# Kernel optimization log

Measured on AMD Instinct MI355X. Metric: run time of the kernel, lower is better.

## Reference

```python
import jax, jax.numpy as jnp
import numpy as np

N, B, M = 262144, 4, 32
C3D, C2D, MID, OUT = 64, 256, 128, 64
H, W = 96, 312
VOXEL_SIZE = jnp.array([0.05, 0.05, 0.1], dtype=jnp.float32)
PC_RANGE = jnp.array([0.0, -40.0, -3.0], dtype=jnp.float32)
CLASS_W3D = jnp.array([0.85, 0.95, 0.6], dtype=jnp.float32)  # Car, Pedestrian, Cyclist
DEFAULT_W3D = 0.8
EPS = 1e-5

def _bn(x, g, b, m, v):
    # eval-mode batchnorm
    return (x - m) * jax.lax.rsqrt(v + EPS) * g + b

def setup_inputs():
    key = jax.random.key(0)
    ks = jax.random.split(key, 16)
    vb = jax.random.randint(ks[0], (N,), 0, B)
    vz = jax.random.randint(ks[1], (N,), 0, 40)
    vy = jax.random.randint(ks[2], (N,), 0, 1600)
    vx = jax.random.randint(ks[3], (N,), 0, 1408)
    voxel_coords = jnp.stack([vb, vz, vy, vx], axis=1).astype(jnp.int32)
    voxel_features = jax.random.normal(ks[4], (N, C3D), dtype=jnp.float32)
    image_features = jax.random.normal(ks[5], (B, C2D, H, W), dtype=jnp.float32)
    cxy = jax.random.uniform(ks[6], (B, M, 2)) * jnp.array([70.4, 80.0]) + jnp.array([0.0, -40.0])
    cz = jax.random.uniform(ks[7], (B, M, 1)) * 4.0 - 3.0
    dims = jax.random.uniform(ks[8], (B, M, 3)) * 3.0 + 1.0
    yaw = jax.random.uniform(ks[9], (B, M, 1)) * 6.28
    gt_boxes = jnp.concatenate([cxy, cz, dims, yaw], axis=-1).astype(jnp.float32)
    gt_classes = jax.random.randint(ks[10], (B, M), 0, 3)
    def lin(k, o, i):
        return (jax.random.normal(k, (o, i), dtype=jnp.float32) / np.float32(np.sqrt(i)))
    return dict(
        voxel_features=voxel_features, voxel_coords=voxel_coords,
        image_features=image_features, gt_boxes=gt_boxes, gt_classes=gt_classes,
        w_vt=lin(ks[11], MID, C3D), b_vt=jnp.zeros(MID),
        g_vt=jnp.ones(MID), be_vt=jnp.zeros(MID), m_vt=jnp.zeros(MID), v_vt=jnp.ones(MID),
        w_it=lin(ks[12], MID, C2D), b_it=jnp.zeros(MID),
        g_it=jnp.ones(MID), be_it=jnp.zeros(MID), m_it=jnp.zeros(MID), v_it=jnp.ones(MID),
        w_f=lin(ks[13], OUT, 2 * MID), b_f=jnp.zeros(OUT),
        g_f=jnp.ones(OUT), be_f=jnp.zeros(OUT), m_f=jnp.zeros(OUT), v_f=jnp.ones(OUT),
    )

def reference(voxel_features, voxel_coords, image_features, gt_boxes, gt_classes,
              w_vt, b_vt, g_vt, be_vt, m_vt, v_vt,
              w_it, b_it, g_it, be_it, m_it, v_it,
              w_f, b_f, g_f, be_f, m_f, v_f):
    b_idx = voxel_coords[:, 0]
    xyz = jnp.stack([voxel_coords[:, 3], voxel_coords[:, 2], voxel_coords[:, 1]], axis=1).astype(jnp.float32)
    centers_raw = xyz * VOXEL_SIZE + PC_RANGE            # class-aware path (no half-voxel offset)
    centers = centers_raw + VOXEL_SIZE * 0.5             # sampling path

    # voxel transform: Linear + BN + ReLU
    vt = jax.nn.relu(_bn(voxel_features @ w_vt.T + b_vt, g_vt, be_vt, m_vt, v_vt))

    # image transform: 1x1 conv + BN + ReLU over all images at once
    it = jnp.einsum('oc,bchw->bohw', w_it, image_features) + b_it[None, :, None, None]
    it = jax.nn.relu(_bn(it, g_it[None, :, None, None], be_it[None, :, None, None],
                         m_it[None, :, None, None], v_it[None, :, None, None]))

    # fallback projection (no calib): xy*10 + [W/2, H/2], normalize to [-1,1], clamp
    px = centers[:, 0] * 10.0 + W / 2.0
    py = centers[:, 1] * 10.0 + H / 2.0
    nx = jnp.clip(px / W * 2.0 - 1.0, -1.0, 1.0)
    ny = jnp.clip(py / H * 2.0 - 1.0, -1.0, 1.0)
    # grid_sample bilinear, align_corners=False, zero padding
    fx = ((nx + 1.0) * W - 1.0) * 0.5
    fy = ((ny + 1.0) * H - 1.0) * 0.5
    x0 = jnp.floor(fx); y0 = jnp.floor(fy)

    def gather(xi, yi):
        valid = (xi >= 0) & (xi < W) & (yi >= 0) & (yi < H)
        xc = jnp.clip(xi, 0, W - 1).astype(jnp.int32)
        yc = jnp.clip(yi, 0, H - 1).astype(jnp.int32)
        return it[b_idx, :, yc, xc] * valid[:, None].astype(it.dtype)  # (N, MID)

    wx1 = (fx - x0)[:, None]; wy1 = (fy - y0)[:, None]
    sampled = (gather(x0, y0) * (1.0 - wx1) * (1.0 - wy1)
             + gather(x0 + 1, y0) * wx1 * (1.0 - wy1)
             + gather(x0, y0 + 1) * (1.0 - wx1) * wy1
             + gather(x0 + 1, y0 + 1) * wx1 * wy1)

    # class-aware weights: axis-aligned point-in-box test; later boxes overwrite earlier
    cen = gt_boxes[..., :3][b_idx]          # (N, M, 3)
    dim = gt_boxes[..., 3:6][b_idx]         # (N, M, 3)
    valid_box = (gt_boxes[..., 3] > 0)[b_idx]  # (N, M)
    inb = jnp.all(jnp.abs(centers_raw[:, None, :] - cen) < dim * 0.5, axis=-1) & valid_box
    any_in = jnp.any(inb, axis=1)
    last = jnp.argmax(jnp.where(inb, jnp.arange(M), -1), axis=1)  # last matching box
    cls = gt_classes[b_idx, last]
    w3d = jnp.where(any_in, CLASS_W3D[cls], DEFAULT_W3D)[:, None]

    fused = jnp.concatenate([vt * w3d, sampled * (1.0 - w3d)], axis=1)
    out = jax.nn.relu(_bn(fused @ w_f.T + b_f, g_f, be_f, m_f, v_f))
    return out
```

## Files before the change

### kernel.cpp

```cpp
#include <hip/hip_runtime.h>

typedef _Float16 half8  __attribute__((ext_vector_type(8)));
typedef _Float16 half4v __attribute__((ext_vector_type(4)));
typedef _Float16 half2v __attribute__((ext_vector_type(2)));
typedef float    f32x4  __attribute__((ext_vector_type(4)));

#define N_VOX  262144
#define BATCH  4
#define NBOX   32
#define C3D_   64
#define C2D_   256
#define MIDC   128
#define OUTC   64
#define IH     96
#define IW     312
#define IHW    (IH*IW)
#define EPSF   1e-5f

#define MFMA16(a,b,c) __builtin_amdgcn_mfma_f32_16x16x32_f16(a,b,c,0,0,0)

__global__ __launch_bounds__(256) void prep_all(
    const int*   __restrict__ coords,
    const float* __restrict__ gtb,
    const int*   __restrict__ gtc,
    const float* __restrict__ w_vt, const float* __restrict__ g_vt,
    const float* __restrict__ v_vt, const float* __restrict__ b_vt,
    const float* __restrict__ be_vt, const float* __restrict__ m_vt,
    const float* __restrict__ w_it, const float* __restrict__ g_it,
    const float* __restrict__ v_it, const float* __restrict__ b_it,
    const float* __restrict__ be_it, const float* __restrict__ m_it,
    const float* __restrict__ w_f, const float* __restrict__ g_f,
    const float* __restrict__ v_f, const float* __restrict__ b_f,
    const float* __restrict__ be_f, const float* __restrict__ m_f,
    _Float16* __restrict__ w_vt_s, _Float16* __restrict__ w_it_s,
    _Float16* __restrict__ w_f1_s, _Float16* __restrict__ w_f2_s,
    float* __restrict__ sb_vt, float* __restrict__ sb_it,
    float* __restrict__ sb_f,  float* __restrict__ w3d_buf)
{
    __shared__ float s_box[BATCH*NBOX*7];
    __shared__ int   s_cls[BATCH*NBOX];
    const int tid = threadIdx.x;
    for (int i = tid; i < BATCH*NBOX*7; i += 256) s_box[i] = gtb[i];
    for (int i = tid; i < BATCH*NBOX;   i += 256) s_cls[i] = gtc[i];
    __syncthreads();

    const int v = blockIdx.x * 256 + tid;

    {
        const int4 cc = ((const int4*)coords)[v];
        const int vb = cc.x;
        const float crx = cc.w * 0.05f;
        const float cry = cc.z * 0.05f - 40.0f;
        const float crz = cc.y * 0.1f  - 3.0f;
        const float* gb = s_box + vb*(NBOX*7);
        int lastm = -1;
        #pragma unroll 8
        for (int m = 0; m < NBOX; ++m) {
            float dx = gb[m*7+3];
            bool in = (fabsf(crx - gb[m*7+0]) < dx * 0.5f) &&
                      (fabsf(cry - gb[m*7+1]) < gb[m*7+4] * 0.5f) &&
                      (fabsf(crz - gb[m*7+2]) < gb[m*7+5] * 0.5f) &&
                      (dx > 0.f);
            if (in) lastm = m;
        }
        float w3 = 0.8f;
        if (lastm >= 0) {
            int cls = s_cls[vb*NBOX + lastm];
            w3 = (cls == 0) ? 0.85f : ((cls == 1) ? 0.95f : 0.6f);
        }
        w3d_buf[v] = w3;
    }

    if (v < MIDC*C3D_) {
        int o = v >> 6;
        float sa = g_vt[o] * rsqrtf(v_vt[o] + EPSF);
        w_vt_s[v] = (_Float16)(w_vt[v] * sa);
    }
    if (v < MIDC*C2D_) {
        int o = v >> 8;
        float sa = g_it[o] * rsqrtf(v_it[o] + EPSF);
        w_it_s[v] = (_Float16)(w_it[v] * sa);
    }
    if (v < OUTC*C2D_) {
        int o = v >> 8, k = v & 255;
        float sa = g_f[o] * rsqrtf(v_f[o] + EPSF);
        float val = w_f[v] * sa;
        if (k < 128) w_f1_s[o*128 + k]       = (_Float16)val;
        else         w_f2_s[o*128 + (k-128)] = (_Float16)val;
    }
    if (v < MIDC) {
        float sa = g_vt[v] * rsqrtf(v_vt[v] + EPSF);
        sb_vt[v] = (b_vt[v] - m_vt[v]) * sa + be_vt[v];
        float si = g_it[v] * rsqrtf(v_it[v] + EPSF);
        sb_it[v] = (b_it[v] - m_it[v]) * si + be_it[v];
    }
    if (v < OUTC) {
        float sa = g_f[v] * rsqrtf(v_f[v] + EPSF);
        sb_f[v] = (b_f[v] - m_f[v]) * sa + be_f[v];
    }
}

__global__ __launch_bounds__(256, 4) void img_transform(
    const float* __restrict__ img,
    const _Float16* __restrict__ w_it_s,
    const _Float16* __restrict__ w_f2_s,
    const float* __restrict__ sb_it,
    _Float16* __restrict__ Jout)
{
    __shared__ __align__(16) _Float16 s_mem[64*136];

    const int p0   = blockIdx.x * 64;
    const int b    = blockIdx.y;
    const int tid  = threadIdx.x;
    const int lane = tid & 63;
    const int wv   = tid >> 6;
    const int r    = lane & 15;
    const int kh   = lane >> 4;

    f32x4 acc[4][2] = {};

    const int p  = tid & 63;
    const int cb = (tid >> 6) * 2;

    const float sbit0 = sb_it[wv*32 + r];
    const float sbit1 = sb_it[wv*32 + 16 + r];

    for (int kc = 0; kc < 4; ++kc) {
        #pragma unroll
        for (int i = 0; i < 8; ++i) {
            int c = cb + i*8;
            float x0 = img[(size_t)(b*C2D_ + kc*64 + c    )*IHW + p0 + p];
            float x1 = img[(size_t)(b*C2D_ + kc*64 + c + 1)*IHW + p0 + p];
            half2v h; h[0] = (_Float16)x0; h[1] = (_Float16)x1;
            *(half2v*)&s_mem[p*72 + c] = h;
        }
        half8 bw[2][2];
        #pragma unroll
        for (int nt = 0; nt < 2; ++nt)
            #pragma unroll
            for (int ks = 0; ks < 2; ++ks) {
                int o = wv*32 + nt*16 + r;
                bw[nt][ks] = *(const half8*)&w_it_s[o*C2D_ + kc*64 + ks*32 + kh*8];
            }
        __syncthreads();
        #pragma unroll
        for (int mt = 0; mt < 4; ++mt)
            #pragma unroll
            for (int ks = 0; ks < 2; ++ks) {
                half8 af = *(const half8*)&s_mem[(mt*16 + r)*72 + ks*32 + kh*8];
                acc[mt][0] = MFMA16(af, bw[0][ks], acc[mt][0]);
                acc[mt][1] = MFMA16(af, bw[1][ks], acc[mt][1]);
            }
        __syncthreads();
    }

    #pragma unroll
    for (int nt = 0; nt < 2; ++nt) {
        int o = wv*32 + nt*16 + r;
        float sb = nt ? sbit1 : sbit0;
        #pragma unroll
        for (int mt = 0; mt < 4; ++mt)
            #pragma unroll
            for (int rr = 0; rr < 4; ++rr) {
                int p2 = mt*16 + kh*4 + rr;
                s_mem[p2*136 + o] = (_Float16)fmaxf(acc[mt][nt][rr] + sb, 0.f);
            }
    }
    __syncthreads();

    {
        const int o2 = wv*16 + r;
        half8 bf2[4];
        #pragma unroll
        for (int ks = 0; ks < 4; ++ks)
            bf2[ks] = *(const half8*)&w_f2_s[o2*128 + ks*32 + kh*8];
        #pragma unroll
        for (int mt = 0; mt < 4; ++mt) {
            f32x4 a2 = {0.f,0.f,0.f,0.f};
            #pragma unroll
            for (int ks = 0; ks < 4; ++ks) {
                half8 af = *(const half8*)&s_mem[(mt*16 + r)*136 + ks*32 + kh*8];
                a2 = MFMA16(af, bf2[ks], a2);
            }
            #pragma unroll
            for (int rr = 0; rr < 4; ++rr) {
                int p2 = mt*16 + kh*4 + rr;
                Jout[(size_t)(b*IHW + p0 + p2)*OUTC + o2] = (_Float16)a2[rr];
            }
        }
    }
}

__global__ __launch_bounds__(256, 4) void voxel_fuse(
    const float* __restrict__ vf,
    const int*   __restrict__ coords,
    const _Float16* __restrict__ w_vt_s,
    const float* __restrict__ sb_vt,
    const _Float16* __restrict__ Jimg,
    const _Float16* __restrict__ w_f1_s,
    const float* __restrict__ sb_f,
    const float* __restrict__ w3d_buf,
    float* __restrict__ out)
{
    __shared__ __align__(16) _Float16 s_vf[64*72];
    __shared__ __align__(16) _Float16 s_fused[64*136];
    __shared__ __align__(16) _Float16 s_j[64*72];
    __shared__ float s_w3d[64];

    const int tid  = threadIdx.x;
    const int lane = tid & 63;
    const int wv   = tid >> 6;
    const int v0   = blockIdx.x * 64;
    const int r    = lane & 15;
    const int kh   = lane >> 4;
    const int vsv  = tid >> 2;
    const int q_   = tid & 3;

    float4 vfr[4];
    {
        const float4* src = (const float4*)(vf + (size_t)(v0 + vsv)*C3D_ + q_*16);
        #pragma unroll
        for (int i = 0; i < 4; ++i) vfr[i] = src[i];
    }
    const float w3 = w3d_buf[v0 + vsv];
    const int4 cc = ((const int4*)coords)[v0 + vsv];

    int ga[4]; float gw[4];
    {
        const int vb = cc.x;
        const float crx = cc.w * 0.05f;
        const float cry = cc.z * 0.05f - 40.0f;
        const float px = (crx + 0.025f) * 10.f + 156.f;
        const float py = (cry + 0.025f) * 10.f + 48.f;
        const float nx = fminf(fmaxf(px / 312.f * 2.f - 1.f, -1.f), 1.f);
        const float ny = fminf(fmaxf(py / 96.f  * 2.f - 1.f, -1.f), 1.f);
        const float fx = ((nx + 1.f) * 312.f - 1.f) * 0.5f;
        const float fy = ((ny + 1.f) * 96.f  - 1.f) * 0.5f;
        const float x0f = floorf(fx), y0f = floorf(fy);
        const float wx1 = fx - x0f, wy1 = fy - y0f;
        const int x0 = (int)x0f, y0 = (int)y0f;
        #pragma unroll
        for (int c = 0; c < 4; ++c) {
            int xi = x0 + (c & 1), yi = y0 + (c >> 1);
            bool valid = (xi >= 0) && (xi < IW) && (yi >= 0) && (yi < IH);
            int xc = min(max(xi, 0), IW - 1);
            int yc = min(max(yi, 0), IH - 1);
            ga[c] = ((vb*IH + yc)*IW + xc) * OUTC;
            float wx = (c & 1) ? wx1 : 1.f - wx1;
            float wy = (c >> 1) ? wy1 : 1.f - wy1;
            gw[c] = valid ? wx * wy : 0.f;
        }
    }

    half8 bvt[2][2];
    float sbvt[2];
    #pragma unroll
    for (int nt = 0; nt < 2; ++nt) {
        int o = (2*wv + nt)*16 + r;
        #pragma unroll
        for (int ks = 0; ks < 2; ++ks)
            bvt[nt][ks] = *(const half8*)&w_vt_s[o*C3D_ + ks*32 + kh*8];
        sbvt[nt] = sb_vt[o];
    }
    const int of = wv*16 + r;
    half8 bf1[4];
    #pragma unroll
    for (int ks = 0; ks < 4; ++ks)
        bf1[ks] = *(const half8*)&w_f1_s[of*128 + ks*32 + kh*8];
    const float sbf = sb_f[of];

    #pragma unroll
    for (int i = 0; i < 4; ++i) {
        float4 x = vfr[i];
        half4v h;
        h[0] = (_Float16)x.x; h[1] = (_Float16)x.y;
        h[2] = (_Float16)x.z; h[3] = (_Float16)x.w;
        *(half4v*)&s_vf[vsv*72 + q_*16 + i*4] = h;
    }
    if (q_ == 0) s_w3d[vsv] = w3;
    __syncthreads();

    half8 jreg[4][2];
    #pragma unroll
    for (int c = 0; c < 4; ++c)
        #pragma unroll
        for (int h = 0; h < 2; ++h)
            jreg[c][h] = *(const half8*)&Jimg[ga[c] + (h*4 + q_)*8];

    #pragma unroll
    for (int mt = 0; mt < 4; ++mt) {
        f32x4 a0 = {0.f,0.f,0.f,0.f}, a1 = {0.f,0.f,0.f,0.f};
        #pragma unroll
        for (int ks = 0; ks < 2; ++ks) {
            half8 af = *(const half8*)&s_vf[(mt*16 + r)*72 + ks*32 + kh*8];
            a0 = MFMA16(af, bvt[0][ks], a0);
            a1 = MFMA16(af, bvt[1][ks], a1);
        }
        #pragma unroll
        for (int rr = 0; rr < 4; ++rr) {
            int v = mt*16 + kh*4 + rr;
            float w3v = s_w3d[v];
            s_fused[v*136 + (2*wv+0)*16 + r] =
                (_Float16)(fmaxf(a0[rr] + sbvt[0], 0.f) * w3v);
            s_fused[v*136 + (2*wv+1)*16 + r] =
                (_Float16)(fmaxf(a1[rr] + sbvt[1], 0.f) * w3v);
        }
    }

    {
        float invw = 1.f - w3;
        #pragma unroll
        for (int h = 0; h < 2; ++h) {
            half8 res;
            #pragma unroll
            for (int i = 0; i < 8; ++i) {
                float s = gw[0]*(float)jreg[0][h][i] + gw[1]*(float)jreg[1][h][i]
                        + gw[2]*(float)jreg[2][h][i] + gw[3]*(float)jreg[3][h][i];
                res[i] = (_Float16)(s * invw);
            }
            *(half8*)&s_j[vsv*72 + (h*4 + q_)*8] = res;
        }
    }
    __syncthreads();

    #pragma unroll
    for (int mt = 0; mt < 4; ++mt) {
        f32x4 acc = {0.f,0.f,0.f,0.f};
        #pragma unroll
        for (int ks = 0; ks < 4; ++ks) {
            half8 af = *(const half8*)&s_fused[(mt*16 + r)*136 + ks*32 + kh*8];
            acc = MFMA16(af, bf1[ks], acc);
        }
        #pragma unroll
        for (int rr = 0; rr < 4; ++rr) {
            int v = mt*16 + kh*4 + rr;
            float jv = (float)s_j[v*72 + of];
            out[(size_t)(v0 + v)*OUTC + of] = fmaxf(acc[rr] + jv + sbf, 0.f);
        }
    }
}

extern "C" void kernel_launch(void* const* d_in, const int* in_sizes, int n_in,
                              void* d_out, int out_size, void* d_ws, size_t ws_size,
                              hipStream_t stream)
{
    const float* vf    = (const float*)d_in[0];
    const int*   vc    = (const int*)  d_in[1];
    const float* img   = (const float*)d_in[2];
    const float* gtb   = (const float*)d_in[3];
    const int*   gtc   = (const int*)  d_in[4];
    const float* w_vt  = (const float*)d_in[5];
    const float* b_vt  = (const float*)d_in[6];
    const float* g_vt  = (const float*)d_in[7];
    const float* be_vt = (const float*)d_in[8];
    const float* m_vt  = (const float*)d_in[9];
    const float* v_vt  = (const float*)d_in[10];
    const float* w_it  = (const float*)d_in[11];
    const float* b_it  = (const float*)d_in[12];
    const float* g_it  = (const float*)d_in[13];
    const float* be_it = (const float*)d_in[14];
    const float* m_it  = (const float*)d_in[15];
    const float* v_it  = (const float*)d_in[16];
    const float* w_f   = (const float*)d_in[17];
    const float* b_f   = (const float*)d_in[18];
    const float* g_f   = (const float*)d_in[19];
    const float* be_f  = (const float*)d_in[20];
    const float* m_f   = (const float*)d_in[21];
    const float* v_f   = (const float*)d_in[22];

    _Float16* ws_h   = (_Float16*)d_ws;
    _Float16* Jbuf   = ws_h;
    _Float16* w_vt_s = ws_h + (size_t)BATCH*IHW*OUTC;
    _Float16* w_it_s = w_vt_s + MIDC*C3D_;
    _Float16* w_f1_s = w_it_s + MIDC*C2D_;
    _Float16* w_f2_s = w_f1_s + OUTC*128;
    float*    fbase  = (float*)(w_f2_s + OUTC*128);
    float* sb_vt   = fbase;
    float* sb_it   = sb_vt + MIDC;
    float* sb_f    = sb_it + MIDC;
    float* w3d_buf = sb_f + OUTC;
    float* outp = (float*)d_out;

    prep_all<<<N_VOX/256, 256, 0, stream>>>(
        vc, gtb, gtc,
        w_vt, g_vt, v_vt, b_vt, be_vt, m_vt,
        w_it, g_it, v_it, b_it, be_it, m_it,
        w_f,  g_f,  v_f,  b_f,  be_f,  m_f,
        w_vt_s, w_it_s, w_f1_s, w_f2_s,
        sb_vt, sb_it, sb_f, w3d_buf);

    img_transform<<<dim3(IHW/64, BATCH), 256, 0, stream>>>(
        img, w_it_s, w_f2_s, sb_it, Jbuf);

    voxel_fuse<<<N_VOX/64, 256, 0, stream>>>(
        vf, vc, w_vt_s, sb_vt, Jbuf, w_f1_s, sb_f, w3d_buf, outp);
}
```

Baseline: 85.81 us.

## Make voxel_fuse wave-independent with per-wave voxel tiles and no block barriers

Each wave now owns 16 voxels and computes all output channels for them, in place of splitting output channels across waves over a shared 64-voxel tile. Voxel features are loaded straight into MFMA A-operand registers, so the s_vf staging buffer and both __syncthreads go away, leaving only wave-private LDS for the fused and image terms. Weights are now loaded from global/L2 inside the output loops rather than held in registers, which adds weight traffic per wave. The occupancy hint is lowered from 4 to 3 blocks per SM. Intra-wave LDS write-then-read happens without an explicit barrier, relying on wave lockstep execution.

Measured after the change: 124.4 us. +44.9%, slower.

```diff
diff --git a/kernel.cpp b/kernel.cpp
--- a/kernel.cpp
+++ b/kernel.cpp
@@ -191,7 +191,7 @@
     }
 }
 
-__global__ __launch_bounds__(256, 4) void voxel_fuse(
+__global__ __launch_bounds__(256, 3) void voxel_fuse(
     const float* __restrict__ vf,
     const int*   __restrict__ coords,
     const _Float16* __restrict__ w_vt_s,
@@ -202,29 +202,28 @@
     const float* __restrict__ w3d_buf,
     float* __restrict__ out)
 {
-    __shared__ __align__(16) _Float16 s_vf[64*72];
-    __shared__ __align__(16) _Float16 s_fused[64*136];
-    __shared__ __align__(16) _Float16 s_j[64*72];
-    __shared__ float s_w3d[64];
+    __shared__ __align__(16) _Float16 s_fused[4][16*136];
+    __shared__ __align__(16) _Float16 s_j[4][16*72];
 
     const int tid  = threadIdx.x;
+    const int w    = tid >> 6;
     const int lane = tid & 63;
-    const int wv   = tid >> 6;
-    const int v0   = blockIdx.x * 64;
     const int r    = lane & 15;
     const int kh   = lane >> 4;
-    const int vsv  = tid >> 2;
-    const int q_   = tid & 3;
-
-    float4 vfr[4];
-    {
-        const float4* src = (const float4*)(vf + (size_t)(v0 + vsv)*C3D_ + q_*16);
-        #pragma unroll
-        for (int i = 0; i < 4; ++i) vfr[i] = src[i];
-    }
-    const float w3 = w3d_buf[v0 + vsv];
-    const int4 cc = ((const int4*)coords)[v0 + vsv];
-
+    const int vj   = lane >> 2;
+    const int q_   = lane & 3;
+    const int vb0  = blockIdx.x * 64 + w * 16;
+
+    _Float16* fused = s_fused[w];
+    _Float16* sj    = s_j[w];
+
+    const float4* vfrow = (const float4*)(vf + (size_t)(vb0 + r)*C3D_);
+    float4 xa0 = vfrow[kh*2];
+    float4 xb0 = vfrow[kh*2 + 1];
+    float4 xa1 = vfrow[8 + kh*2];
+    float4 xb1 = vfrow[8 + kh*2 + 1];
+
+    const int4 cc = ((const int4*)coords)[vb0 + vj];
     int ga[4]; float gw[4];
     {
         const int vb = cc.x;
@@ -252,34 +251,6 @@
         }
     }
 
-    half8 bvt[2][2];
-    float sbvt[2];
-    #pragma unroll
-    for (int nt = 0; nt < 2; ++nt) {
-        int o = (2*wv + nt)*16 + r;
-        #pragma unroll
-        for (int ks = 0; ks < 2; ++ks)
-            bvt[nt][ks] = *(const half8*)&w_vt_s[o*C3D_ + ks*32 + kh*8];
-        sbvt[nt] = sb_vt[o];
-    }
-    const int of = wv*16 + r;
-    half8 bf1[4];
-    #pragma unroll
-    for (int ks = 0; ks < 4; ++ks)
-        bf1[ks] = *(const half8*)&w_f1_s[of*128 + ks*32 + kh*8];
-    const float sbf = sb_f[of];
-
-    #pragma unroll
-    for (int i = 0; i < 4; ++i) {
-        float4 x = vfr[i];
-        half4v h;
-        h[0] = (_Float16)x.x; h[1] = (_Float16)x.y;
-        h[2] = (_Float16)x.z; h[3] = (_Float16)x.w;
-        *(half4v*)&s_vf[vsv*72 + q_*16 + i*4] = h;
-    }
-    if (q_ == 0) s_w3d[vsv] = w3;
-    __syncthreads();
-
     half8 jreg[4][2];
     #pragma unroll
     for (int c = 0; c < 4; ++c)
@@ -287,55 +258,68 @@
         for (int h = 0; h < 2; ++h)
             jreg[c][h] = *(const half8*)&Jimg[ga[c] + (h*4 + q_)*8];
 
-    #pragma unroll
-    for (int mt = 0; mt < 4; ++mt) {
-        f32x4 a0 = {0.f,0.f,0.f,0.f}, a1 = {0.f,0.f,0.f,0.f};
-        #pragma unroll
-        for (int ks = 0; ks < 2; ++ks) {
-            half8 af = *(const half8*)&s_vf[(mt*16 + r)*72 + ks*32 + kh*8];
-            a0 = MFMA16(af, bvt[0][ks], a0);
-            a1 = MFMA16(af, bvt[1][ks], a1);
-        }
+    const float4 w3v = *(const float4*)&w3d_buf[vb0 + kh*4];
+    const float invw = 1.f - w3d_buf[vb0 + vj];
+
+    half8 af0, af1;
+    af0[0]=(_Float16)xa0.x; af0[1]=(_Float16)xa0.y;
+    af0[2]=(_Float16)xa0.z; af0[3]=(_Float16)xa0.w;
+    af0[4]=(_Float16)xb0.x; af0[5]=(_Float16)xb0.y;
+    af0[6]=(_Float16)xb0.z; af0[7]=(_Float16)xb0.w;
+    af1[0]=(_Float16)xa1.x; af1[1]=(_Float16)xa1.y;
+    af1[2]=(_Float16)xa1.z; af1[3]=(_Float16)xa1.w;
+    af1[4]=(_Float16)xb1.x; af1[5]=(_Float16)xb1.y;
+    af1[6]=(_Float16)xb1.z; af1[7]=(_Float16)xb1.w;
+
+    #pragma unroll
+    for (int ot = 0; ot < 8; ++ot) {
+        const int o = ot*16 + r;
+        half8 b0 = *(const half8*)&w_vt_s[o*C3D_ + kh*8];
+        half8 b1 = *(const half8*)&w_vt_s[o*C3D_ + 32 + kh*8];
+        f32x4 a = {0.f,0.f,0.f,0.f};
+        a = MFMA16(af0, b0, a);
+        a = MFMA16(af1, b1, a);
+        const float sb = sb_vt[o];
         #pragma unroll
         for (int rr = 0; rr < 4; ++rr) {
-            int v = mt*16 + kh*4 + rr;
-            float w3v = s_w3d[v];
-            s_fused[v*136 + (2*wv+0)*16 + r] =
-                (_Float16)(fmaxf(a0[rr] + sbvt[0], 0.f) * w3v);
-            s_fused[v*136 + (2*wv+1)*16 + r] =
-                (_Float16)(fmaxf(a1[rr] + sbvt[1], 0.f) * w3v);
-        }
-    }
-
-    {
-        float invw = 1.f - w3;
-        #pragma unroll
-        for (int h = 0; h < 2; ++h) {
-            half8 res;
-            #pragma unroll
-            for (int i = 0; i < 8; ++i) {
-                float s = gw[0]*(float)jreg[0][h][i] + gw[1]*(float)jreg[1][h][i]
-                        + gw[2]*(float)jreg[2][h][i] + gw[3]*(float)jreg[3][h][i];
-                res[i] = (_Float16)(s * invw);
-            }
-            *(half8*)&s_j[vsv*72 + (h*4 + q_)*8] = res;
-        }
-    }
-    __syncthreads();
-
-    #pragma unroll
-    for (int mt = 0; mt < 4; ++mt) {
-        f32x4 acc = {0.f,0.f,0.f,0.f};
+            int vloc = kh*4 + rr;
+            fused[vloc*136 + ot*16 + r] =
+                (_Float16)(fmaxf(a[rr] + sb, 0.f) * w3v[rr]);
+        }
+    }
+
+    #pragma unroll
+    for (int h = 0; h < 2; ++h) {
+        half8 res;
+        #pragma unroll
+        for (int i = 0; i < 8; ++i) {
+            float s = gw[0]*(float)jreg[0][h][i] + gw[1]*(float)jreg[1][h][i]
+                    + gw[2]*(float)jreg[2][h][i] + gw[3]*(float)jreg[3][h][i];
+            res[i] = (_Float16)(s * invw);
+        }
+        *(half8*)&sj[vj*72 + (h*4 + q_)*8] = res;
+    }
+
+    half8 af2[4];
+    #pragma unroll
+    for (int ks = 0; ks < 4; ++ks)
+        af2[ks] = *(const half8*)&fused[r*136 + ks*32 + kh*8];
+
+    #pragma unroll
+    for (int ot = 0; ot < 4; ++ot) {
+        const int o = ot*16 + r;
+        f32x4 a = {0.f,0.f,0.f,0.f};
         #pragma unroll
         for (int ks = 0; ks < 4; ++ks) {
-            half8 af = *(const half8*)&s_fused[(mt*16 + r)*136 + ks*32 + kh*8];
-            acc = MFMA16(af, bf1[ks], acc);
-        }
+            half8 b = *(const half8*)&w_f1_s[o*128 + ks*32 + kh*8];
+            a = MFMA16(af2[ks], b, a);
+        }
+        const float sb = sb_f[o];
         #pragma unroll
         for (int rr = 0; rr < 4; ++rr) {
-            int v = mt*16 + kh*4 + rr;
-            float jv = (float)s_j[v*72 + of];
-            out[(size_t)(v0 + v)*OUTC + of] = fmaxf(acc[rr] + jv + sbf, 0.f);
+            int vloc = kh*4 + rr;
+            float jv = (float)sj[vloc*72 + o];
+            out[(size_t)(vb0 + vloc)*OUTC + o] = fmaxf(a[rr] + jv + sb, 0.f);
         }
     }
 }
```
